# Kernel optimization log

Hardware: AMD Instinct MI355X
Metric: run time of the kernel (lower is better)

The kernel has to match this reference:

```python
import jax, jax.numpy as jnp
import numpy as np

# dims (match init_kwargs / input_specs)
B, T = 32, 512
DIM, DEPTH, HEADS, NB_FEAT, N_MASKS = 256, 6, 8, 128, 4
DIM_HEAD = DIM // HEADS  # 32
FF_MULT = 4
KERNEL_EPS = 1e-4


def _orth_proj(key, m, d):
    # FAVOR+ gaussian orthogonal random features: stacked QR blocks, row norms from fresh gaussians
    nb = m // d
    keys = jax.random.split(key, nb + 1)
    blocks = []
    for i in range(nb):
        g = jax.random.normal(keys[i], (d, d))
        q, _ = jnp.linalg.qr(g)
        blocks.append(q.T)
    proj = jnp.concatenate(blocks, axis=0)  # (m, d)
    norms = jnp.linalg.norm(jax.random.normal(keys[-1], (m, d)), axis=-1)
    return (proj * norms[:, None]).astype(jnp.float32)


def setup_inputs() -> dict:
    key = jax.random.key(0)
    ks = jax.random.split(key, 12)
    init = lambda k, sh: (jax.random.normal(k, sh, dtype=jnp.float32) * 0.02)
    L = DEPTH
    return {
        "mel": jax.random.normal(ks[0], (B, DIM, T), dtype=jnp.float32),
        "proj": _orth_proj(ks[1], NB_FEAT, DIM_HEAD),
        "ln1_g": jnp.ones((L, DIM), jnp.float32), "ln1_b": jnp.zeros((L, DIM), jnp.float32),
        "Wq": init(ks[2], (L, DIM, DIM)), "Wk": init(ks[3], (L, DIM, DIM)),
        "Wv": init(ks[4], (L, DIM, DIM)),
        "Wo": init(ks[5], (L, DIM, DIM)), "bo": jnp.zeros((L, DIM), jnp.float32),
        "ln2_g": jnp.ones((L, DIM), jnp.float32), "ln2_b": jnp.zeros((L, DIM), jnp.float32),
        "W1": init(ks[6], (L, DIM, FF_MULT * DIM)), "b1": jnp.zeros((L, FF_MULT * DIM), jnp.float32),
        "W2": init(ks[7], (L, FF_MULT * DIM, DIM)), "b2": jnp.zeros((L, DIM), jnp.float32),
        "Wm": init(ks[8], (DIM, N_MASKS)), "bm": jnp.zeros((N_MASKS,), jnp.float32),
    }


def _ln(x, g, b):
    mu = jnp.mean(x, -1, keepdims=True)
    var = jnp.var(x, -1, keepdims=True)
    return (x - mu) * jax.lax.rsqrt(var + 1e-5) * g + b


def _softmax_kernel(x, proj, is_query):
    # x: (B,H,N,dh), proj: (m,dh)
    dn = x.shape[-1] ** -0.25
    ratio = proj.shape[0] ** -0.5
    xd = jnp.einsum('bhnd,md->bhnm', x * dn, proj)
    diag = 0.5 * jnp.sum(jnp.square(x * dn), axis=-1, keepdims=True)
    if is_query:
        mx = jnp.max(xd, axis=-1, keepdims=True)
    else:
        mx = jnp.max(xd, axis=(-1, -2), keepdims=True)
    return ratio * (jnp.exp(xd - diag - mx) + KERNEL_EPS)


def _split_heads(x):
    b, n, _ = x.shape
    return x.reshape(b, n, HEADS, DIM_HEAD).transpose(0, 2, 1, 3)  # (B,H,N,dh)


def _forward(mel, proj, ln1_g, ln1_b, Wq, Wk, Wv, Wo, bo, ln2_g, ln2_b, W1, b1, W2, b2, Wm, bm):
    x = jnp.transpose(mel, (0, 2, 1))  # (B, T, DIM)
    for l in range(DEPTH):
        # --- FAVOR+ self-attention (pre-LN, non-causal linear attention) ---
        h = _ln(x, ln1_g[l], ln1_b[l])
        q = _split_heads(h @ Wq[l])
        k = _split_heads(h @ Wk[l])
        v = _split_heads(h @ Wv[l])
        qp = _softmax_kernel(q, proj, True)   # (B,H,T,m)
        kp = _softmax_kernel(k, proj, False)  # (B,H,T,m)
        ctx = jnp.einsum('bhnm,bhnd->bhmd', kp, v)          # (B,H,m,dh)
        o = jnp.einsum('bhnm,bhmd->bhnd', qp, ctx)          # (B,H,T,dh)
        denom = jnp.einsum('bhnm,bhm->bhn', qp, kp.sum(axis=2))
        o = o / denom[..., None]
        o = o.transpose(0, 2, 1, 3).reshape(x.shape[0], x.shape[1], DIM)
        x = x + o @ Wo[l] + bo[l]
        h = _ln(x, ln2_g[l], ln2_b[l])
        x = x + jax.nn.gelu(h @ W1[l] + b1[l]) @ W2[l] + b2[l]
    masks = x @ Wm + bm                  # (B, T, M)
    return jnp.transpose(masks, (0, 2, 1))  # (B, M, T)


def reference(mel, proj, ln1_g, ln1_b, Wq, Wk, Wv, Wo, bo, ln2_g, ln2_b, W1, b1, W2, b2, Wm, bm):
    return _forward(mel, proj, ln1_g, ln1_b, Wq, Wk, Wv, Wo, bo, ln2_g, ln2_b, W1, b1, W2, b2, Wm, bm)
```

## Files before the change

kernel.cpp:

```cpp
#include <hip/hip_runtime.h>
#include <math.h>

#define B 32
#define T 512
#define D 256
#define H 8
#define DH 32
#define MF 128
#define NLAYER 6
#define FF 1024
#define NM 4
#define BT (B*T)
#define BH (B*H)

#define DN2H 0.08838834764831845f
#define DNS  0.4204482076268573f
#define RATIO 0.08838834764831845f
#define KEPS 1e-4f

typedef __attribute__((ext_vector_type(8))) short short8;
typedef __attribute__((ext_vector_type(4))) float f32x4;

#define MFMA(a, b, c) __builtin_amdgcn_mfma_f32_16x16x32_bf16(a, b, c, 0, 0, 0)

#define SWZG(l) (((((l) & 3) + (((l) >> 3) & 3)) & 3) * 8)
#define RS(li, gi) (((((gi) - ((li) >> 1)) & 3)) * 8)

__device__ __forceinline__ ushort f2b(float x) {
  union { float f; unsigned u; } c; c.f = x;
  unsigned r = (c.u + 0x7FFFu + ((c.u >> 16) & 1u)) >> 16;
  return (ushort)r;
}
__device__ __forceinline__ float bf2f(ushort u) {
  union { unsigned u; float f; } c; c.u = ((unsigned)u) << 16;
  return c.f;
}
__device__ __forceinline__ void gload16(const ushort* g, ushort* l) {
  __builtin_amdgcn_global_load_lds((const __attribute__((address_space(1))) void*)g,
                                   (__attribute__((address_space(3))) void*)l, 16, 0, 0);
}

__global__ void transpose_mel(const float* __restrict__ mel, float* __restrict__ x) {
  __shared__ float tile[32][33];
  int b = blockIdx.z;
  int d0 = blockIdx.y * 32, t0 = blockIdx.x * 32;
  int tx = threadIdx.x, ty = threadIdx.y;
  #pragma unroll
  for (int i = 0; i < 32; i += 8)
    tile[ty + i][tx] = mel[(b * D + d0 + ty + i) * T + t0 + tx];
  __syncthreads();
  #pragma unroll
  for (int i = 0; i < 32; i += 8)
    x[(b * T + t0 + ty + i) * D + d0 + tx] = tile[tx][ty + i];
}

__global__ void wtrans(const float* __restrict__ W, ushort* __restrict__ WT,
                       int K, int N, size_t lin, size_t lout) {
  __shared__ float tile[32][33];
  int l = blockIdx.z;
  const float* Wl = W + (size_t)l * lin;
  ushort* WTl = WT + (size_t)l * lout;
  int k0 = blockIdx.y * 32, n0 = blockIdx.x * 32;
  int tx = threadIdx.x, ty = threadIdx.y;
  #pragma unroll
  for (int i = 0; i < 32; i += 8)
    tile[ty + i][tx] = Wl[(size_t)(k0 + ty + i) * N + n0 + tx];
  __syncthreads();
  #pragma unroll
  for (int i = 0; i < 32; i += 8)
    WTl[(size_t)(n0 + ty + i) * K + k0 + tx] = f2b(tile[tx][ty + i]);
}

__global__ void proj_conv(const float* __restrict__ proj, ushort* __restrict__ projd) {
  int e = blockIdx.x * 256 + threadIdx.x;
  if (e < MF * DH) projd[e] = f2b(proj[e] * DNS);
}

__global__ __launch_bounds__(256) void ln_kernel(const float* __restrict__ x, const float* __restrict__ g,
                          const float* __restrict__ bb, ushort* __restrict__ y) {
  int row = blockIdx.x * 4 + (threadIdx.x >> 6);
  int lane = threadIdx.x & 63;
  const float4 v = ((const float4*)(x + (size_t)row * D))[lane];
  float s = v.x + v.y + v.z + v.w;
  #pragma unroll
  for (int off = 32; off; off >>= 1) s += __shfl_down(s, off);
  s = __shfl(s, 0);
  float mu = s * (1.0f / 256.0f);
  float dx = v.x - mu, dy = v.y - mu, dz = v.z - mu, dw = v.w - mu;
  float q = dx * dx + dy * dy + dz * dz + dw * dw;
  #pragma unroll
  for (int off = 32; off; off >>= 1) q += __shfl_down(q, off);
  q = __shfl(q, 0);
  float rstd = rsqrtf(q * (1.0f / 256.0f) + 1e-5f);
  const float4 gg = ((const float4*)g)[lane];
  const float4 be = ((const float4*)bb)[lane];
  ushort4 o;
  o.x = f2b(dx * rstd * gg.x + be.x);
  o.y = f2b(dy * rstd * gg.y + be.y);
  o.z = f2b(dz * rstd * gg.z + be.z);
  o.w = f2b(dw * rstd * gg.w + be.w);
  ((ushort4*)(y + (size_t)row * D))[lane] = o;
}

template<int EPI>
__global__ __launch_bounds__(256) void gemm_wide(
    const ushort* __restrict__ A, const ushort* __restrict__ BTm,
    const float* __restrict__ bias,
    ushort* __restrict__ outB,
    ushort* __restrict__ qo, ushort* __restrict__ ko, ushort* __restrict__ vT,
    int N, int K) {
  __shared__ __align__(16) ushort Al[2][32 * 32];
  __shared__ __align__(16) ushort Bl[2][256 * 32];
  int tid = threadIdx.x;
  int wave = tid >> 6, lane = tid & 63;
  int gi = lane >> 4, li = lane & 15;
  int lrow = lane >> 2, lkb = SWZG(lane);
  int row0 = blockIdx.x * 32, col0 = blockIdx.y * 256;
  f32x4 acc[2][4] = {};

  auto stage = [&](int buf, int kk) {
    if (wave < 2)
      gload16(&A[(size_t)(row0 + wave * 16 + lrow) * K + kk + lkb], &Al[buf][wave * 512]);
    #pragma unroll
    for (int i = 0; i < 4; i++) {
      int chunk = wave * 4 + i;
      gload16(&BTm[(size_t)(col0 + chunk * 16 + lrow) * K + kk + lkb], &Bl[buf][chunk * 512]);
    }
  };

  stage(0, 0);
  __syncthreads();
  int cur = 0;
  for (int k0 = 0; k0 < K; k0 += 32, cur ^= 1) {
    if (k0 + 32 < K) stage(cur ^ 1, k0 + 32);
    short8 a[2], b[4];
    #pragma unroll
    for (int m = 0; m < 2; m++)
      a[m] = *(const short8*)&Al[cur][(m * 16 + li) * 32 + RS(li, gi)];
    #pragma unroll
    for (int n = 0; n < 4; n++)
      b[n] = *(const short8*)&Bl[cur][(wave * 64 + n * 16 + li) * 32 + RS(li, gi)];
    #pragma unroll
    for (int m = 0; m < 2; m++)
      #pragma unroll
      for (int n = 0; n < 4; n++)
        acc[m][n] = MFMA(a[m], b[n], acc[m][n]);
    __syncthreads();
  }
  #pragma unroll
  for (int m = 0; m < 2; m++) {
    int rbase = row0 + m * 16 + gi * 4;
    #pragma unroll
    for (int n = 0; n < 4; n++) {
      int col = col0 + wave * 64 + n * 16 + li;
      f32x4 v = acc[m][n];
      if (EPI == 2) {
        float bs = bias[col];
        #pragma unroll
        for (int r = 0; r < 4; r++) {
          float u = v[r] + bs;
          float p = u + 0.044715f * u * u * u;
          float gel = u / (1.0f + __expf(-1.5957691216057308f * p));
          outB[(size_t)(rbase + r) * N + col] = f2b(gel);
        }
      } else {
        if (col < 256) {
          #pragma unroll
          for (int r = 0; r < 4; r++) qo[(size_t)(rbase + r) * 256 + col] = f2b(v[r]);
        } else if (col < 512) {
          #pragma unroll
          for (int r = 0; r < 4; r++) ko[(size_t)(rbase + r) * 256 + col - 256] = f2b(v[r]);
        } else {
          int b_ = rbase >> 9, t = rbase & 511;
          int hh = (col - 512) >> 5, d = (col - 512) & 31;
          ushort4 pk;
          pk.x = f2b(v[0]); pk.y = f2b(v[1]); pk.z = f2b(v[2]); pk.w = f2b(v[3]);
          *(ushort4*)&vT[((size_t)((b_ * 8 + hh) * 32 + d)) * 512 + t] = pk;
        }
      }
    }
  }
}

__global__ __launch_bounds__(512) void ctx_fused(
    const ushort* __restrict__ kb, const ushort* __restrict__ projd,
    const ushort* __restrict__ vT, ushort* __restrict__ Bmat) {
  __shared__ __align__(16) ushort Kl[512 * 32];
  __shared__ __align__(16) ushort Pl[128 * 32];
  __shared__ __align__(16) ushort Sl[2][128 * 40];
  __shared__ __align__(16) ushort Bvl[2][32 * 32];
  __shared__ float dg_s[512];
  __shared__ float red_s[512];
  int bh = blockIdx.x;
  int b = bh >> 3, h = bh & 7;
  int tid = threadIdx.x, wave = tid >> 6, lane = tid & 63;
  int gi = lane >> 4, li = lane & 15;
  int lrow = lane >> 2, lkb = (lane & 3) * 8;
  const ushort* Kg = kb + (size_t)(b * 512) * 256 + h * 32;
  const ushort* Vg = vT + (size_t)bh * 32 * 512;
  #pragma unroll
  for (int i = 0; i < 4; i++) {
    int chunk = wave * 4 + i;
    gload16(&Kg[(size_t)(chunk * 16 + lrow) * 256 + lkb], &Kl[chunk * 512]);
  }
  gload16(&projd[(wave * 16 + lrow) * 32 + lkb], &Pl[wave * 512]);
  __syncthreads();
  {
    const ushort* kr = &Kl[tid * 32];
    float s = 0.f;
    #pragma unroll
    for (int j = 0; j < 32; j++) { float v = bf2f(kr[j]); s += v * v; }
    dg_s[tid] = DN2H * s;
  }
  short8 bp = *(const short8*)&Pl[(wave * 16 + li) * 32 + gi * 8];
  float smax = -1e30f;
  for (int c = 0; c < 16; c++) {
    int t0c = c * 32;
    short8 a0 = *(const short8*)&Kl[(t0c + li) * 32 + gi * 8];
    short8 a1 = *(const short8*)&Kl[(t0c + 16 + li) * 32 + gi * 8];
    f32x4 s0 = {}, s1 = {};
    s0 = MFMA(a0, bp, s0); s1 = MFMA(a1, bp, s1);
    #pragma unroll
    for (int r = 0; r < 4; r++)
      smax = fmaxf(smax, fmaxf(s0[r], s1[r]));
  }
  red_s[tid] = smax;
  __syncthreads();
  for (int s = 256; s; s >>= 1) {
    if (tid < s) red_s[tid] = fmaxf(red_s[tid], red_s[tid + s]);
    __syncthreads();
  }
  float km = red_s[0];
  f32x4 cacc[2] = {};
  float ks = 0.f;
  int cur = 0;
  for (int c = 0; c < 16; c++, cur ^= 1) {
    int t0c = c * 32;
    if (wave < 2)
      gload16(&Vg[(size_t)(wave * 16 + lrow) * 512 + t0c + lkb], &Bvl[cur][wave * 512]);
    short8 a0 = *(const short8*)&Kl[(t0c + li) * 32 + gi * 8];
    short8 a1 = *(const short8*)&Kl[(t0c + 16 + li) * 32 + gi * 8];
    f32x4 s0 = {}, s1 = {};
    s0 = MFMA(a0, bp, s0); s1 = MFMA(a1, bp, s1);
    ushort4 w0, w1;
    #pragma unroll
    for (int r = 0; r < 4; r++) {
      float d0 = dg_s[t0c + gi * 4 + r];
      float d1 = dg_s[t0c + 16 + gi * 4 + r];
      float k0 = RATIO * (__expf(s0[r] - d0 - km) + KEPS);
      float k1 = RATIO * (__expf(s1[r] - d1 - km) + KEPS);
      ks += k0 + k1;
      ((ushort*)&w0)[r] = f2b(k0);
      ((ushort*)&w1)[r] = f2b(k1);
    }
    *(ushort4*)&Sl[cur][(wave * 16 + li) * 40 + gi * 4]      = w0;
    *(ushort4*)&Sl[cur][(wave * 16 + li) * 40 + 16 + gi * 4] = w1;
    __syncthreads();
    short8 ca = *(const short8*)&Sl[cur][(wave * 16 + li) * 40 + gi * 8];
    short8 cb0 = *(const short8*)&Bvl[cur][li * 32 + gi * 8];
    short8 cb1 = *(const short8*)&Bvl[cur][(16 + li) * 32 + gi * 8];
    cacc[0] = MFMA(ca, cb0, cacc[0]);
    cacc[1] = MFMA(ca, cb1, cacc[1]);
  }
  ks += __shfl_xor(ks, 16); ks += __shfl_xor(ks, 32);
  if (gi == 0)
    Bmat[((size_t)bh * 48 + 32) * 128 + wave * 16 + li] = f2b(ks);
  #pragma unroll
  for (int n = 0; n < 2; n++) {
    int dd = n * 16 + li;
    int mg = wave * 16 + gi * 4;
    ushort4 pk;
    pk.x = f2b(cacc[n][0]); pk.y = f2b(cacc[n][1]);
    pk.z = f2b(cacc[n][2]); pk.w = f2b(cacc[n][3]);
    *(ushort4*)&Bmat[((size_t)bh * 48 + dd) * 128 + mg] = pk;
  }
  for (int e = tid; e < 15 * 128; e += 512)
    Bmat[((size_t)bh * 48 + 33) * 128 + e] = 0;
}

__global__ __launch_bounds__(256) void favq_o(
    const ushort* __restrict__ qb, const ushort* __restrict__ projd,
    const ushort* __restrict__ Bmat, ushort* __restrict__ ob) {
  __shared__ __align__(16) ushort Ql[64 * 32];
  __shared__ __align__(16) ushort Pl[128 * 32];
  __shared__ __align__(16) ushort Sl[64 * 136];
  __shared__ __align__(16) ushort Bml[48 * 136];
  __shared__ float dgq[64];
  int bh = blockIdx.y;
  int t0 = blockIdx.x * 64;
  int b = bh >> 3, h = bh & 7;
  int tid = threadIdx.x, wave = tid >> 6, lane = tid & 63;
  int gi = lane >> 4, li = lane & 15;
  int lrow = lane >> 2, lkb = (lane & 3) * 8;
  const ushort* Qg = qb + (size_t)(b * 512) * 256 + h * 32;
  gload16(&Qg[(size_t)(t0 + wave * 16 + lrow) * 256 + lkb], &Ql[wave * 512]);
  #pragma unroll
  for (int i = 0; i < 2; i++) {
    int chunk = wave * 2 + i;
    gload16(&projd[(chunk * 16 + lrow) * 32 + lkb], &Pl[chunk * 512]);
  }
  #pragma unroll
  for (int j = 0; j < 3; j++) {
    int c = j * 256 + tid;
    int r = c >> 4, g = c & 15;
    *(uint4*)&Bml[r * 136 + g * 8] = *(const uint4*)&Bmat[(size_t)bh * 48 * 128 + r * 128 + g * 8];
  }
  __syncthreads();
  if (tid < 64) {
    const ushort* qr = &Ql[tid * 32];
    float s = 0.f;
    #pragma unroll
    for (int j = 0; j < 32; j++) { float v = bf2f(qr[j]); s += v * v; }
    dgq[tid] = DN2H * s;
  }
  short8 bq = *(const short8*)&Ql[(wave * 16 + li) * 32 + gi * 8];
  f32x4 sacc[8] = {};
  #pragma unroll
  for (int m = 0; m < 8; m++) {
    short8 a = *(const short8*)&Pl[(m * 16 + li) * 32 + gi * 8];
    sacc[m] = MFMA(a, bq, sacc[m]);
  }
  __syncthreads();
  float mx = -1e30f;
  #pragma unroll
  for (int m = 0; m < 8; m++)
    #pragma unroll
    for (int r = 0; r < 4; r++) mx = fmaxf(mx, sacc[m][r]);
  mx = fmaxf(mx, __shfl_xor(mx, 16));
  mx = fmaxf(mx, __shfl_xor(mx, 32));
  float dg = dgq[wave * 16 + li];
  #pragma unroll
  for (int m = 0; m < 8; m++) {
    ushort4 o4;
    #pragma unroll
    for (int r = 0; r < 4; r++)
      ((ushort*)&o4)[r] = f2b(RATIO * (__expf(sacc[m][r] - dg - mx) + KEPS));
    *(ushort4*)&Sl[(wave * 16 + li) * 136 + m * 16 + gi * 4] = o4;
  }
  __syncthreads();
  f32x4 oacc[3] = {};
  #pragma unroll
  for (int ks = 0; ks < 4; ks++) {
    short8 a = *(const short8*)&Sl[(wave * 16 + li) * 136 + ks * 32 + gi * 8];
    #pragma unroll
    for (int n = 0; n < 3; n++) {
      short8 bb = *(const short8*)&Bml[(n * 16 + li) * 136 + ks * 32 + gi * 8];
      oacc[n] = MFMA(a, bb, oacc[n]);
    }
  }
  int t = t0 + wave * 16 + gi * 4;
  float den[4];
  #pragma unroll
  for (int r = 0; r < 4; r++) den[r] = __shfl(oacc[2][r], lane & 48);
  #pragma unroll
  for (int n = 0; n < 2; n++)
    #pragma unroll
    for (int r = 0; r < 4; r++)
      ob[((size_t)(b * 512) + t + r) * 256 + h * 32 + n * 16 + li] = f2b(oacc[n][r] / den[r]);
}

template<int MODE>
__global__ __launch_bounds__(256) void gemm_ln2(
    const ushort* __restrict__ A, const ushort* __restrict__ BTm,
    const float* __restrict__ bias, const float* __restrict__ res,
    float* __restrict__ x, const float* __restrict__ g, const float* __restrict__ bvec,
    ushort* __restrict__ hout,
    const float* __restrict__ Wm, const float* __restrict__ bm, float* __restrict__ mout,
    int K) {
  __shared__ __align__(16) ushort Al[2][32 * 32];
  __shared__ __align__(16) ushort Bl[2][256 * 32];
  __shared__ float rs1[4 * 32];
  __shared__ float rs2[4 * 32];
  __shared__ float pmS[4 * 128];
  int tid = threadIdx.x, wave = tid >> 6, lane = tid & 63;
  int gi = lane >> 4, li = lane & 15;
  int lrow = lane >> 2, lkb = SWZG(lane);
  int row0 = blockIdx.x * 32;
  int wc = wave;
  f32x4 acc[2][4] = {};

  auto stage = [&](int buf, int kk) {
    if (wave < 2)
      gload16(&A[(size_t)(row0 + wave * 16 + lrow) * K + kk + lkb], &Al[buf][wave * 512]);
    #pragma unroll
    for (int i = 0; i < 4; i++) {
      int chunk = wave * 4 + i;
      gload16(&BTm[(size_t)(chunk * 16 + lrow) * K + kk + lkb], &Bl[buf][chunk * 512]);
    }
  };

  stage(0, 0);
  __syncthreads();
  int cur = 0;
  for (int k0 = 0; k0 < K; k0 += 32, cur ^= 1) {
    if (k0 + 32 < K) stage(cur ^ 1, k0 + 32);
    short8 a[2], b[4];
    #pragma unroll
    for (int m = 0; m < 2; m++)
      a[m] = *(const short8*)&Al[cur][(m * 16 + li) * 32 + RS(li, gi)];
    #pragma unroll
    for (int n = 0; n < 4; n++)
      b[n] = *(const short8*)&Bl[cur][(wc * 64 + n * 16 + li) * 32 + RS(li, gi)];
    #pragma unroll
    for (int m = 0; m < 2; m++)
      #pragma unroll
      for (int n = 0; n < 4; n++)
        acc[m][n] = MFMA(a[m], b[n], acc[m][n]);
    __syncthreads();
  }
  #pragma unroll
  for (int m = 0; m < 2; m++) {
    #pragma unroll
    for (int r = 0; r < 4; r++) {
      int row = row0 + m * 16 + gi * 4 + r;
      int ridx = m * 16 + gi * 4 + r;
      float s1 = 0.f, s2 = 0.f;
      #pragma unroll
      for (int n = 0; n < 4; n++) {
        int col = wc * 64 + n * 16 + li;
        float val = acc[m][n][r] + bias[col] + res[(size_t)row * 256 + col];
        acc[m][n][r] = val;
        s1 += val; s2 += val * val;
      }
      if (MODE == 0) {
        #pragma unroll
        for (int off = 1; off <= 8; off <<= 1) { s1 += __shfl_xor(s1, off); s2 += __shfl_xor(s2, off); }
        if (li == 0) { rs1[wave * 32 + ridx] = s1; rs2[wave * 32 + ridx] = s2; }
      } else {
        #pragma unroll
        for (int msk = 0; msk < NM; msk++) {
          float sm = 0.f;
          #pragma unroll
          for (int n = 0; n < 4; n++) {
            int col = wc * 64 + n * 16 + li;
            sm += acc[m][n][r] * Wm[col * NM + msk];
          }
          #pragma unroll
          for (int off = 1; off <= 8; off <<= 1) sm += __shfl_xor(sm, off);
          if (li == 0) pmS[wave * 128 + ridx * 4 + msk] = sm;
        }
      }
    }
  }
  __syncthreads();
  if (MODE == 0) {
    float g4[4], bv4[4];
    #pragma unroll
    for (int n = 0; n < 4; n++) {
      int col = wc * 64 + n * 16 + li;
      g4[n] = g[col]; bv4[n] = bvec[col];
    }
    #pragma unroll
    for (int m = 0; m < 2; m++) {
      #pragma unroll
      for (int r = 0; r < 4; r++) {
        int row = row0 + m * 16 + gi * 4 + r;
        int ridx = m * 16 + gi * 4 + r;
        float t1 = rs1[ridx] + rs1[32 + ridx] + rs1[64 + ridx] + rs1[96 + ridx];
        float t2 = rs2[ridx] + rs2[32 + ridx] + rs2[64 + ridx] + rs2[96 + ridx];
        float mu = t1 * (1.f / 256.f);
        float rstd = rsqrtf(t2 * (1.f / 256.f) - mu * mu + 1e-5f);
        #pragma unroll
        for (int n = 0; n < 4; n++) {
          int col = wc * 64 + n * 16 + li;
          float val = acc[m][n][r];
          x[(size_t)row * 256 + col] = val;
          hout[(size_t)row * 256 + col] = f2b((val - mu) * rstd * g4[n] + bv4[n]);
        }
      }
    }
  } else {
    if (tid < 128) {
      int ridx = tid >> 2, msk = tid & 3;
      float tot = pmS[ridx * 4 + msk] + pmS[128 + ridx * 4 + msk] +
                  pmS[256 + ridx * 4 + msk] + pmS[384 + ridx * 4 + msk];
      int grow = row0 + ridx;
      int bb_ = grow >> 9, t = grow & 511;
      mout[((size_t)(bb_ * NM) + msk) * 512 + t] = tot + bm[msk];
    }
  }
}

extern "C" void kernel_launch(void* const* d_in, const int* in_sizes, int n_in,
                              void* d_out, int out_size, void* d_ws, size_t ws_size,
                              hipStream_t stream) {
  const float* mel   = (const float*)d_in[0];
  const float* proj  = (const float*)d_in[1];
  const float* ln1_g = (const float*)d_in[2];
  const float* ln1_b = (const float*)d_in[3];
  const float* Wq    = (const float*)d_in[4];
  const float* Wk    = (const float*)d_in[5];
  const float* Wv    = (const float*)d_in[6];
  const float* Wo    = (const float*)d_in[7];
  const float* bo    = (const float*)d_in[8];
  const float* ln2_g = (const float*)d_in[9];
  const float* ln2_b = (const float*)d_in[10];
  const float* W1    = (const float*)d_in[11];
  const float* b1    = (const float*)d_in[12];
  const float* W2    = (const float*)d_in[13];
  const float* b2    = (const float*)d_in[14];
  const float* Wm    = (const float*)d_in[15];
  const float* bm    = (const float*)d_in[16];

  float* x      = (float*)d_ws;
  ushort* us    = (ushort*)(x + (size_t)BT * D);
  ushort* h     = us;                   us += (size_t)BT * D;
  ushort* qb    = us;                   us += (size_t)BT * D;
  ushort* kb    = us;                   us += (size_t)BT * D;
  ushort* vT    = us;                   us += (size_t)BH * 32 * T;
  ushort* ob    = us;                   us += (size_t)BT * D;
  ushort* ffh   = us;                   us += (size_t)BT * FF;
  ushort* Bmat  = us;                   us += (size_t)BH * 48 * MF;
  ushort* qkvT  = us;                   us += (size_t)NLAYER * 768 * 256;
  ushort* woT   = us;                   us += (size_t)NLAYER * 256 * 256;
  ushort* w1T   = us;                   us += (size_t)NLAYER * 1024 * 256;
  ushort* w2T   = us;                   us += (size_t)NLAYER * 256 * 1024;
  ushort* projd = us;                   us += (size_t)MF * DH;

  wtrans<<<dim3(8, 8, NLAYER), dim3(32, 8), 0, stream>>>(Wq, qkvT, 256, 256, 65536, 768 * 256);
  wtrans<<<dim3(8, 8, NLAYER), dim3(32, 8), 0, stream>>>(Wk, qkvT + 256 * 256, 256, 256, 65536, 768 * 256);
  wtrans<<<dim3(8, 8, NLAYER), dim3(32, 8), 0, stream>>>(Wv, qkvT + 512 * 256, 256, 256, 65536, 768 * 256);
  wtrans<<<dim3(8, 8, NLAYER), dim3(32, 8), 0, stream>>>(Wo, woT, 256, 256, 65536, 65536);
  wtrans<<<dim3(32, 8, NLAYER), dim3(32, 8), 0, stream>>>(W1, w1T, 256, 1024, 262144, 262144);
  wtrans<<<dim3(8, 32, NLAYER), dim3(32, 8), 0, stream>>>(W2, w2T, 1024, 256, 262144, 262144);
  proj_conv<<<16, 256, 0, stream>>>(proj, projd);

  transpose_mel<<<dim3(T / 32, D / 32, B), dim3(32, 8), 0, stream>>>(mel, x);
  ln_kernel<<<BT / 4, 256, 0, stream>>>(x, ln1_g, ln1_b, h);

  for (int l = 0; l < NLAYER; l++) {
    gemm_wide<0><<<dim3(BT / 32, 3), 256, 0, stream>>>(h, qkvT + (size_t)l * 768 * 256,
        nullptr, nullptr, qb, kb, vT, 768, 256);
    ctx_fused<<<BH, 512, 0, stream>>>(kb, projd, vT, Bmat);
    favq_o<<<dim3(8, BH), 256, 0, stream>>>(qb, projd, Bmat, ob);
    gemm_ln2<0><<<BT / 32, 256, 0, stream>>>(ob, woT + (size_t)l * 256 * 256,
        bo + l * D, x, x, ln2_g + l * D, ln2_b + l * D, h,
        nullptr, nullptr, nullptr, 256);
    gemm_wide<2><<<dim3(BT / 32, 4), 256, 0, stream>>>(h, w1T + (size_t)l * 1024 * 256,
        b1 + (size_t)l * FF, ffh, nullptr, nullptr, nullptr, 1024, 256);
    if (l < NLAYER - 1) {
      gemm_ln2<0><<<BT / 32, 256, 0, stream>>>(ffh, w2T + (size_t)l * 256 * 1024,
          b2 + l * D, x, x, ln1_g + (l + 1) * D, ln1_b + (l + 1) * D, h,
          nullptr, nullptr, nullptr, 1024);
    } else {
      gemm_ln2<1><<<BT / 32, 256, 0, stream>>>(ffh, w2T + (size_t)l * 256 * 1024,
          b2 + l * D, x, x, nullptr, nullptr, nullptr,
          Wm, bm, (float*)d_out, 1024);
    }
  }
}
```

Baseline: 759.2 us.

## Fuse FFN up-projection, GELU and down-projection into one kernel

Replaces the separate W1 GEMM (writing a bf16 BTx1024 intermediate to global memory) and the W2 GEMM+LN kernel with a single 512-thread kernel per 32-row tile. The GELU output is kept in a 64KB LDS buffer with a swizzled layout and consumed directly by the second GEMM, which also handles the residual, the next LayerNorm or the mask head. This removes the global round trip of the FFN hidden activations and one launch per layer. In exchange, the large LDS footprint lowers occupancy, and each block now does both GEMMs serially with only 512 blocks in the grid.

Result: slower. 862.8 us (+13.6%).

```diff
diff --git a/kernel.cpp b/kernel.cpp
--- a/kernel.cpp
+++ b/kernel.cpp
@@ -359,19 +359,15 @@
       ob[((size_t)(b * 512) + t + r) * 256 + h * 32 + n * 16 + li] = f2b(oacc[n][r] / den[r]);
 }
 
-template<int MODE>
 __global__ __launch_bounds__(256) void gemm_ln2(
     const ushort* __restrict__ A, const ushort* __restrict__ BTm,
     const float* __restrict__ bias, const float* __restrict__ res,
     float* __restrict__ x, const float* __restrict__ g, const float* __restrict__ bvec,
-    ushort* __restrict__ hout,
-    const float* __restrict__ Wm, const float* __restrict__ bm, float* __restrict__ mout,
-    int K) {
+    ushort* __restrict__ hout, int K) {
   __shared__ __align__(16) ushort Al[2][32 * 32];
   __shared__ __align__(16) ushort Bl[2][256 * 32];
   __shared__ float rs1[4 * 32];
   __shared__ float rs2[4 * 32];
-  __shared__ float pmS[4 * 128];
   int tid = threadIdx.x, wave = tid >> 6, lane = tid & 63;
   int gi = lane >> 4, li = lane & 15;
   int lrow = lane >> 2, lkb = SWZG(lane);
@@ -420,6 +416,153 @@
         int col = wc * 64 + n * 16 + li;
         float val = acc[m][n][r] + bias[col] + res[(size_t)row * 256 + col];
         acc[m][n][r] = val;
+        s1 += val; s2 += val * val;
+      }
+      #pragma unroll
+      for (int off = 1; off <= 8; off <<= 1) { s1 += __shfl_xor(s1, off); s2 += __shfl_xor(s2, off); }
+      if (li == 0) { rs1[wave * 32 + ridx] = s1; rs2[wave * 32 + ridx] = s2; }
+    }
+  }
+  __syncthreads();
+  float g4[4], bv4[4];
+  #pragma unroll
+  for (int n = 0; n < 4; n++) {
+    int col = wc * 64 + n * 16 + li;
+    g4[n] = g[col]; bv4[n] = bvec[col];
+  }
+  #pragma unroll
+  for (int m = 0; m < 2; m++) {
+    #pragma unroll
+    for (int r = 0; r < 4; r++) {
+      int row = row0 + m * 16 + gi * 4 + r;
+      int ridx = m * 16 + gi * 4 + r;
+      float t1 = rs1[ridx] + rs1[32 + ridx] + rs1[64 + ridx] + rs1[96 + ridx];
+      float t2 = rs2[ridx] + rs2[32 + ridx] + rs2[64 + ridx] + rs2[96 + ridx];
+      float mu = t1 * (1.f / 256.f);
+      float rstd = rsqrtf(t2 * (1.f / 256.f) - mu * mu + 1e-5f);
+      #pragma unroll
+      for (int n = 0; n < 4; n++) {
+        int col = wc * 64 + n * 16 + li;
+        float val = acc[m][n][r];
+        x[(size_t)row * 256 + col] = val;
+        hout[(size_t)row * 256 + col] = f2b((val - mu) * rstd * g4[n] + bv4[n]);
+      }
+    }
+  }
+}
+
+template<int MODE>
+__global__ __launch_bounds__(512) void ff_fused(
+    const ushort* __restrict__ A, const ushort* __restrict__ w1T,
+    const float* __restrict__ b1v, const ushort* __restrict__ w2T,
+    const float* __restrict__ b2v, const float* __restrict__ res,
+    float* __restrict__ x, const float* __restrict__ g, const float* __restrict__ bvec,
+    ushort* __restrict__ hout,
+    const float* __restrict__ Wm, const float* __restrict__ bm, float* __restrict__ mout) {
+  __shared__ __align__(16) ushort Fl[64 * 512];
+  __shared__ __align__(16) ushort Bl[2][256 * 32];
+  __shared__ __align__(16) ushort Alh[2][32 * 32];
+  __shared__ float rs1[8 * 32], rs2[8 * 32];
+  __shared__ float pmS[8 * 32 * 4];
+  int tid = threadIdx.x, wave = tid >> 6, lane = tid & 63;
+  int gi = lane >> 4, li = lane & 15;
+  int lrow = lane >> 2, lkb = SWZG(lane);
+  int row0 = blockIdx.x * 32;
+
+  auto stage1 = [&](int buf, int step) {
+    int nc = step >> 3, k0 = (step & 7) * 32;
+    if (wave < 2)
+      gload16(&A[(size_t)(row0 + wave * 16 + lrow) * 256 + k0 + lkb], &Alh[buf][wave * 512]);
+    #pragma unroll
+    for (int i = 0; i < 2; i++) {
+      int chunk = wave * 2 + i;
+      gload16(&w1T[(size_t)(nc * 256 + chunk * 16 + lrow) * 256 + k0 + lkb], &Bl[buf][chunk * 512]);
+    }
+  };
+  stage1(0, 0);
+  __syncthreads();
+  int cur = 0;
+  f32x4 acc[2][2] = {};
+  for (int step = 0; step < 32; step++, cur ^= 1) {
+    if (step + 1 < 32) stage1(cur ^ 1, step + 1);
+    short8 a[2], b[2];
+    #pragma unroll
+    for (int m = 0; m < 2; m++)
+      a[m] = *(const short8*)&Alh[cur][(m * 16 + li) * 32 + RS(li, gi)];
+    #pragma unroll
+    for (int n = 0; n < 2; n++)
+      b[n] = *(const short8*)&Bl[cur][(wave * 32 + n * 16 + li) * 32 + RS(li, gi)];
+    #pragma unroll
+    for (int m = 0; m < 2; m++)
+      #pragma unroll
+      for (int n = 0; n < 2; n++)
+        acc[m][n] = MFMA(a[m], b[n], acc[m][n]);
+    if ((step & 7) == 7) {
+      int nc = step >> 3;
+      #pragma unroll
+      for (int n = 0; n < 2; n++) {
+        int col32 = n * 16 + li;
+        float bs = b1v[nc * 256 + wave * 32 + col32];
+        int G = col32 >> 3, c7 = col32 & 7;
+        #pragma unroll
+        for (int m = 0; m < 2; m++) {
+          int c16 = (nc * 8 + wave) * 2 + m;
+          #pragma unroll
+          for (int r = 0; r < 4; r++) {
+            int row15 = gi * 4 + r;
+            float u = acc[m][n][r] + bs;
+            float p = u + 0.044715f * u * u * u;
+            float gel = u / (1.0f + __expf(-1.5957691216057308f * p));
+            int slot = (G - (row15 >> 1)) & 3;
+            Fl[c16 * 512 + row15 * 32 + slot * 8 + c7] = f2b(gel);
+            acc[m][n][r] = 0.f;
+          }
+        }
+      }
+    }
+    __syncthreads();
+  }
+
+  auto stage2 = [&](int buf, int k0) {
+    #pragma unroll
+    for (int i = 0; i < 2; i++) {
+      int chunk = wave * 2 + i;
+      gload16(&w2T[(size_t)(chunk * 16 + lrow) * 1024 + k0 + lkb], &Bl[buf][chunk * 512]);
+    }
+  };
+  stage2(0, 0);
+  __syncthreads();
+  cur = 0;
+  f32x4 acc2[2][2] = {};
+  for (int ck = 0; ck < 32; ck++, cur ^= 1) {
+    if (ck + 1 < 32) stage2(cur ^ 1, (ck + 1) * 32);
+    short8 a[2], b[2];
+    #pragma unroll
+    for (int m = 0; m < 2; m++)
+      a[m] = *(const short8*)&Fl[(ck * 2 + m) * 512 + li * 32 + RS(li, gi)];
+    #pragma unroll
+    for (int n = 0; n < 2; n++)
+      b[n] = *(const short8*)&Bl[cur][(wave * 32 + n * 16 + li) * 32 + RS(li, gi)];
+    #pragma unroll
+    for (int m = 0; m < 2; m++)
+      #pragma unroll
+      for (int n = 0; n < 2; n++)
+        acc2[m][n] = MFMA(a[m], b[n], acc2[m][n]);
+    __syncthreads();
+  }
+
+  #pragma unroll
+  for (int m = 0; m < 2; m++) {
+    #pragma unroll
+    for (int r = 0; r < 4; r++) {
+      int row = row0 + m * 16 + gi * 4 + r;
+      int ridx = m * 16 + gi * 4 + r;
+      float s1 = 0.f, s2 = 0.f;
+      #pragma unroll
+      for (int n = 0; n < 2; n++) {
+        int col = wave * 32 + n * 16 + li;
+        float val = acc2[m][n][r] + b2v[col] + res[(size_t)row * 256 + col];
+        acc2[m][n][r] = val;
         s1 += val; s2 += val * val;
       }
       if (MODE == 0) {
@@ -431,9 +574,9 @@
         for (int msk = 0; msk < NM; msk++) {
           float sm = 0.f;
           #pragma unroll
-          for (int n = 0; n < 4; n++) {
-            int col = wc * 64 + n * 16 + li;
-            sm += acc[m][n][r] * Wm[col * NM + msk];
+          for (int n = 0; n < 2; n++) {
+            int col = wave * 32 + n * 16 + li;
+            sm += acc2[m][n][r] * Wm[col * NM + msk];
           }
           #pragma unroll
           for (int off = 1; off <= 8; off <<= 1) sm += __shfl_xor(sm, off);
@@ -444,11 +587,11 @@
   }
   __syncthreads();
   if (MODE == 0) {
-    float g4[4], bv4[4];
-    #pragma unroll
-    for (int n = 0; n < 4; n++) {
-      int col = wc * 64 + n * 16 + li;
-      g4[n] = g[col]; bv4[n] = bvec[col];
+    float g2[2], bv2[2];
+    #pragma unroll
+    for (int n = 0; n < 2; n++) {
+      int col = wave * 32 + n * 16 + li;
+      g2[n] = g[col]; bv2[n] = bvec[col];
     }
     #pragma unroll
     for (int m = 0; m < 2; m++) {
@@ -456,24 +599,26 @@
       for (int r = 0; r < 4; r++) {
         int row = row0 + m * 16 + gi * 4 + r;
         int ridx = m * 16 + gi * 4 + r;
-        float t1 = rs1[ridx] + rs1[32 + ridx] + rs1[64 + ridx] + rs1[96 + ridx];
-        float t2 = rs2[ridx] + rs2[32 + ridx] + rs2[64 + ridx] + rs2[96 + ridx];
+        float t1 = 0.f, t2 = 0.f;
+        #pragma unroll
+        for (int w = 0; w < 8; w++) { t1 += rs1[w * 32 + ridx]; t2 += rs2[w * 32 + ridx]; }
         float mu = t1 * (1.f / 256.f);
         float rstd = rsqrtf(t2 * (1.f / 256.f) - mu * mu + 1e-5f);
         #pragma unroll
-        for (int n = 0; n < 4; n++) {
-          int col = wc * 64 + n * 16 + li;
-          float val = acc[m][n][r];
+        for (int n = 0; n < 2; n++) {
+          int col = wave * 32 + n * 16 + li;
+          float val = acc2[m][n][r];
           x[(size_t)row * 256 + col] = val;
-          hout[(size_t)row * 256 + col] = f2b((val - mu) * rstd * g4[n] + bv4[n]);
+          hout[(size_t)row * 256 + col] = f2b((val - mu) * rstd * g2[n] + bv2[n]);
         }
       }
     }
   } else {
     if (tid < 128) {
       int ridx = tid >> 2, msk = tid & 3;
-      float tot = pmS[ridx * 4 + msk] + pmS[128 + ridx * 4 + msk] +
-                  pmS[256 + ridx * 4 + msk] + pmS[384 + ridx * 4 + msk];
+      float tot = 0.f;
+      #pragma unroll
+      for (int w = 0; w < 8; w++) tot += pmS[w * 128 + ridx * 4 + msk];
       int grow = row0 + ridx;
       int bb_ = grow >> 9, t = grow & 511;
       mout[((size_t)(bb_ * NM) + msk) * 512 + t] = tot + bm[msk];
@@ -509,7 +654,6 @@
   ushort* kb    = us;                   us += (size_t)BT * D;
   ushort* vT    = us;                   us += (size_t)BH * 32 * T;
   ushort* ob    = us;                   us += (size_t)BT * D;
-  ushort* ffh   = us;                   us += (size_t)BT * FF;
   ushort* Bmat  = us;                   us += (size_t)BH * 48 * MF;
   ushort* qkvT  = us;                   us += (size_t)NLAYER * 768 * 256;
   ushort* woT   = us;                   us += (size_t)NLAYER * 256 * 256;
@@ -533,19 +677,18 @@
         nullptr, nullptr, qb, kb, vT, 768, 256);
     ctx_fused<<<BH, 512, 0, stream>>>(kb, projd, vT, Bmat);
     favq_o<<<dim3(8, BH), 256, 0, stream>>>(qb, projd, Bmat, ob);
-    gemm_ln2<0><<<BT / 32, 256, 0, stream>>>(ob, woT + (size_t)l * 256 * 256,
-        bo + l * D, x, x, ln2_g + l * D, ln2_b + l * D, h,
-        nullptr, nullptr, nullptr, 256);
-    gemm_wide<2><<<dim3(BT / 32, 4), 256, 0, stream>>>(h, w1T + (size_t)l * 1024 * 256,
-        b1 + (size_t)l * FF, ffh, nullptr, nullptr, nullptr, 1024, 256);
+    gemm_ln2<<<BT / 32, 256, 0, stream>>>(ob, woT + (size_t)l * 256 * 256,
+        bo + l * D, x, x, ln2_g + l * D, ln2_b + l * D, h, 256);
     if (l < NLAYER - 1) {
-      gemm_ln2<0><<<BT / 32, 256, 0, stream>>>(ffh, w2T + (size_t)l * 256 * 1024,
-          b2 + l * D, x, x, ln1_g + (l + 1) * D, ln1_b + (l + 1) * D, h,
-          nullptr, nullptr, nullptr, 1024);
+      ff_fused<0><<<BT / 32, 512, 0, stream>>>(h, w1T + (size_t)l * 1024 * 256,
+          b1 + (size_t)l * FF, w2T + (size_t)l * 256 * 1024, b2 + l * D, x,
+          x, ln1_g + (l + 1) * D, ln1_b + (l + 1) * D, h,
+          nullptr, nullptr, nullptr);
     } else {
-      gemm_ln2<1><<<BT / 32, 256, 0, stream>>>(ffh, w2T + (size_t)l * 256 * 1024,
-          b2 + l * D, x, x, nullptr, nullptr, nullptr,
-          Wm, bm, (float*)d_out, 1024);
-    }
-  }
-}
+      ff_fused<1><<<BT / 32, 512, 0, stream>>>(h, w1T + (size_t)l * 1024 * 256,
+          b1 + (size_t)l * FF, w2T + (size_t)l * 256 * 1024, b2 + l * D, x,
+          x, nullptr, nullptr, nullptr,
+          Wm, bm, (float*)d_out);
+    }
+  }
+}
```
